# Kernel optimization log

Hardware: AMD Instinct MI355X
Metric: run time of the kernel (lower is better)

The kernel has to match this reference:

```python
import jax, jax.numpy as jnp
import numpy as np
from math import factorial

L_MAX = 3
K = 256
N = 2048


def _cg_coeff(l1, m1, l2, m2, l3, m3):
    # Clebsch-Gordan coefficient <l1 m1 l2 m2 | l3 m3> via the Racah formula.
    if m3 != m1 + m2:
        return 0.0
    pref = ((2 * l3 + 1) * factorial(l3 + l1 - l2) * factorial(l3 - l1 + l2)
            * factorial(l1 + l2 - l3) / factorial(l1 + l2 + l3 + 1)) ** 0.5
    pref *= (factorial(l3 + m3) * factorial(l3 - m3) * factorial(l1 - m1)
             * factorial(l1 + m1) * factorial(l2 - m2) * factorial(l2 + m2)) ** 0.5
    s = 0.0
    for k in range(0, l1 + l2 - l3 + 1):
        d = [k, l1 + l2 - l3 - k, l1 - m1 - k, l2 + m2 - k,
             l3 - l2 + m1 + k, l3 - l1 - m2 + k]
        if min(d) < 0:
            continue
        den = 1.0
        for x in d:
            den *= factorial(x)
        s += (-1.0) ** k / den
    return pref * s


def _cg_tensor(l1, l2, l3):
    out = np.zeros((2 * l1 + 1, 2 * l2 + 1, 2 * l3 + 1), dtype=np.float32)
    for m1 in range(-l1, l1 + 1):
        for m2 in range(-l2, l2 + 1):
            m3 = m1 + m2
            if -l3 <= m3 <= l3:
                out[m1 + l1, m2 + l2, m3 + l3] = _cg_coeff(l1, m1, l2, m2, l3, m3)
    return jnp.asarray(out)


# All (l1, l2) -> l coupling paths allowed by the triangle inequality, l <= L_MAX.
PATHS = {l: [(l1, l2) for l1 in range(L_MAX + 1) for l2 in range(L_MAX + 1)
             if abs(l1 - l2) <= l <= l1 + l2] for l in range(L_MAX + 1)}
CG = {(l1, l2, l): _cg_tensor(l1, l2, l)
      for l in range(L_MAX + 1) for (l1, l2) in PATHS[l]}


def _forward(f1, f2, U, W):
    outs = []
    for l in range(L_MAX + 1):
        # CG tensor product: elementwise over channels k, coupled over (m1, m2) -> m.
        parts = [jnp.einsum('abm,nak,nbk->nmk', CG[(l1, l2, l)], f1[l1], f2[l2])
                 for (l1, l2) in PATHS[l]]
        tp = jnp.concatenate(parts, axis=-1)          # [N, 2l+1, n_paths(l)*K]
        mixed = jnp.einsum('nmc,ck->nmk', tp, U[l])   # U_dict per-l mixing -> [N, 2l+1, K]
        mixed = jnp.einsum('nmk,kj->nmj', mixed, W[l])  # learned per-l linear
        outs.append(f1[l] + mixed)                    # residual
    return tuple(outs)


def setup_inputs() -> dict:
    key = jax.random.key(0)
    ks = jax.random.split(key, 16)
    inp = {}
    for l in range(L_MAX + 1):
        inp[f'f1_l{l}'] = jax.random.normal(ks[l], (N, 2 * l + 1, K), jnp.float32)
        inp[f'f2_l{l}'] = jax.random.normal(ks[4 + l], (N, 2 * l + 1, K), jnp.float32)
        cin = len(PATHS[l]) * K
        inp[f'U_{l}'] = jax.random.normal(ks[8 + l], (cin, K), jnp.float32) / float(np.sqrt(cin))
        inp[f'W_{l}'] = jax.random.normal(ks[12 + l], (K, K), jnp.float32) / float(np.sqrt(K))
    return inp


def reference(f1_l0, f1_l1, f1_l2, f1_l3,
              f2_l0, f2_l1, f2_l2, f2_l3,
              U_0, U_1, U_2, U_3,
              W_0, W_1, W_2, W_3):
    f1 = [f1_l0, f1_l1, f1_l2, f1_l3]
    f2 = [f2_l0, f2_l1, f2_l2, f2_l3]
    U = [U_0, U_1, U_2, U_3]
    W = [W_0, W_1, W_2, W_3]
    return _forward(f1, f2, U, W)
```

## Files before the change

kernel.cpp:

```cpp
#include <hip/hip_runtime.h>
#include <math.h>

typedef __attribute__((ext_vector_type(4))) float f32x4;
typedef __attribute__((ext_vector_type(8))) __bf16 bf16x8;
typedef __attribute__((ext_vector_type(4))) __bf16 bf16x4;

__device__ __constant__ int GP_L[34]  = {0,0,0,0, 1,1,1,1,1,1,1,1,1, 2,2,2,2,2,2,2,2,2,2,2, 3,3,3,3,3,3,3,3,3,3};
__device__ __constant__ int GP_L1[34] = {0,1,2,3, 0,1,1,1,2,2,2,3,3, 0,1,1,1,2,2,2,2,3,3,3, 0,1,1,2,2,2,3,3,3,3};
__device__ __constant__ int GP_L2[34] = {0,1,2,3, 1,0,1,2,1,2,3,2,3, 2,1,2,3,0,1,2,3,1,2,3, 3,2,3,1,2,3,0,1,2,3};

__device__ double dfact(int n) { double r = 1.0; for (int i = 2; i <= n; ++i) r *= (double)i; return r; }

__device__ double cg_coeff(int l1, int m1, int l2, int m2, int l3, int m3) {
  if (m3 != m1 + m2) return 0.0;
  double pref = sqrt((2.0 * l3 + 1.0) * dfact(l3 + l1 - l2) * dfact(l3 - l1 + l2)
                     * dfact(l1 + l2 - l3) / dfact(l1 + l2 + l3 + 1));
  pref *= sqrt(dfact(l3 + m3) * dfact(l3 - m3) * dfact(l1 - m1) * dfact(l1 + m1)
               * dfact(l2 - m2) * dfact(l2 + m2));
  double s = 0.0;
  for (int k = 0; k <= l1 + l2 - l3; ++k) {
    int d0 = k, d1 = l1 + l2 - l3 - k, d2 = l1 - m1 - k, d3 = l2 + m2 - k;
    int d4 = l3 - l2 + m1 + k, d5 = l3 - l1 - m2 + k;
    if (d0 < 0 || d1 < 0 || d2 < 0 || d3 < 0 || d4 < 0 || d5 < 0) continue;
    double den = dfact(d0) * dfact(d1) * dfact(d2) * dfact(d3) * dfact(d4) * dfact(d5);
    s += ((k & 1) ? -1.0 : 1.0) / den;
  }
  return pref * s;
}

__global__ void cg_init(float* __restrict__ cg) {
  int idx = blockIdx.x * 256 + threadIdx.x;
  if (idx >= 34 * 49) return;
  int gp = idx / 49, r = idx % 49;
  int m1i = r / 7, m2i = r % 7;
  int l3 = GP_L[gp], l1 = GP_L1[gp], l2 = GP_L2[gp];
  float v = 0.f;
  if (m1i <= 2 * l1 && m2i <= 2 * l2) {
    int m1 = m1i - l1, m2 = m2i - l2, m3 = m1 + m2;
    if (m3 >= -l3 && m3 <= l3) v = (float)cg_coeff(l1, m1, l2, m2, l3, m3);
  }
  cg[idx] = v;
}

__global__ __launch_bounds__(256) void cvt_u_all(
    const float* __restrict__ u0, const float* __restrict__ u1,
    const float* __restrict__ u2, const float* __restrict__ u3,
    __bf16* __restrict__ out) {
  long i = (long)blockIdx.x * 256 + threadIdx.x;
  const long b1 = 65536, b2 = 212992, b3 = 393216;
  const float* src; long s;
  if (i < b1)      { src = u0; s = i; }
  else if (i < b2) { src = u1; s = i - b1; }
  else if (i < b3) { src = u2; s = i - b2; }
  else             { src = u3; s = i - b3; }
  float4 v = ((const float4*)src)[s];
  bf16x4 o;
  o[0] = (__bf16)v.x; o[1] = (__bf16)v.y; o[2] = (__bf16)v.z; o[3] = (__bf16)v.w;
  ((bf16x4*)out)[i] = o;
}

__global__ void wt_cvt_all(const float* __restrict__ w0, const float* __restrict__ w1,
                           const float* __restrict__ w2, const float* __restrict__ w3,
                           __bf16* __restrict__ Wt) {
  int b = blockIdx.x;
  int l = b >> 8, j = b & 255, k = threadIdx.x;
  const float* W = (l == 0) ? w0 : (l == 1) ? w1 : (l == 2) ? w2 : w3;
  Wt[((long)l << 16) + (j << 8) + k] = (__bf16)W[(k << 8) + j];
}

template <int l1, int l2, int L>
__device__ __forceinline__ void tp_path2(const float* __restrict__ v1, const float* __restrict__ v2,
                                         const float* __restrict__ cgt, float* __restrict__ tp) {
#pragma unroll
  for (int a = 0; a < 2 * l1 + 1; ++a) {
#pragma unroll
    for (int b = 0; b < 2 * l2 + 1; ++b) {
      int mi = a + b - l1 - l2 + L;
      if (mi >= 0 && mi <= 2 * L)
        tp[mi] = fmaf(cgt[a * 7 + b], v1[a] * v2[b], tp[mi]);
    }
  }
}

#define TPW(LV, DST, CIN, GOFF, P, L1V, L2V)                                    \
  { float tp[2 * (LV) + 1] = {};                                                \
    tp_path2<L1V, L2V, LV>(v1 + CUM[L1V], v2 + CUM[L2V], cg + ((GOFF) + (P)) * 49, tp); \
    __bf16* o = (DST) + (n * (2 * (LV) + 1)) * (CIN) + (P) * 256 + k;           \
    _Pragma("unroll")                                                           \
    for (int m = 0; m < 2 * (LV) + 1; ++m) o[(long)m * (CIN)] = (__bf16)tp[m]; }

template <int LMASK>
__global__ __launch_bounds__(256) void tp_all(
    const float* __restrict__ f10, const float* __restrict__ f11,
    const float* __restrict__ f12, const float* __restrict__ f13,
    const float* __restrict__ f20, const float* __restrict__ f21,
    const float* __restrict__ f22, const float* __restrict__ f23,
    const float* __restrict__ cg,
    __bf16* __restrict__ A0, __bf16* __restrict__ A1,
    __bf16* __restrict__ A2, __bf16* __restrict__ A3) {
  const long n = blockIdx.x;
  const int k = threadIdx.x;
  constexpr int CUM[4] = {0, 1, 4, 9};
  const float* f1s[4] = {f10, f11, f12, f13};
  const float* f2s[4] = {f20, f21, f22, f23};

  float v1[16], v2[16];
#pragma unroll
  for (int l1 = 0; l1 < 4; ++l1) {
    const float* p1 = f1s[l1] + (n * (2 * l1 + 1)) * 256 + k;
    const float* p2 = f2s[l1] + (n * (2 * l1 + 1)) * 256 + k;
#pragma unroll
    for (int a = 0; a < 2 * l1 + 1; ++a) {
      v1[CUM[l1] + a] = p1[(long)a * 256];
      v2[CUM[l1] + a] = p2[(long)a * 256];
    }
  }

  if constexpr (LMASK & 1) {
    TPW(0, A0, 1024, 0, 0, 0, 0)  TPW(0, A0, 1024, 0, 1, 1, 1)
    TPW(0, A0, 1024, 0, 2, 2, 2)  TPW(0, A0, 1024, 0, 3, 3, 3)
  }
  if constexpr (LMASK & 2) {
    TPW(1, A1, 2304, 4, 0, 0, 1)  TPW(1, A1, 2304, 4, 1, 1, 0)
    TPW(1, A1, 2304, 4, 2, 1, 1)  TPW(1, A1, 2304, 4, 3, 1, 2)
    TPW(1, A1, 2304, 4, 4, 2, 1)  TPW(1, A1, 2304, 4, 5, 2, 2)
    TPW(1, A1, 2304, 4, 6, 2, 3)  TPW(1, A1, 2304, 4, 7, 3, 2)
    TPW(1, A1, 2304, 4, 8, 3, 3)
  }
  if constexpr (LMASK & 4) {
    TPW(2, A2, 2816, 13, 0, 0, 2)  TPW(2, A2, 2816, 13, 1, 1, 1)
    TPW(2, A2, 2816, 13, 2, 1, 2)  TPW(2, A2, 2816, 13, 3, 1, 3)
    TPW(2, A2, 2816, 13, 4, 2, 0)  TPW(2, A2, 2816, 13, 5, 2, 1)
    TPW(2, A2, 2816, 13, 6, 2, 2)  TPW(2, A2, 2816, 13, 7, 2, 3)
    TPW(2, A2, 2816, 13, 8, 3, 1)  TPW(2, A2, 2816, 13, 9, 3, 2)
    TPW(2, A2, 2816, 13, 10, 3, 3)
  }
  if constexpr (LMASK & 8) {
    TPW(3, A3, 2560, 24, 0, 0, 3)  TPW(3, A3, 2560, 24, 1, 1, 2)
    TPW(3, A3, 2560, 24, 2, 1, 3)  TPW(3, A3, 2560, 24, 3, 2, 1)
    TPW(3, A3, 2560, 24, 4, 2, 2)  TPW(3, A3, 2560, 24, 5, 2, 3)
    TPW(3, A3, 2560, 24, 6, 3, 0)  TPW(3, A3, 2560, 24, 7, 3, 1)
    TPW(3, A3, 2560, 24, 8, 3, 2)  TPW(3, A3, 2560, 24, 9, 3, 3)
  }
}

struct GemmDesc {
  const __bf16* A[4];
  const __bf16* B[4];
  void*         C[4];
  const float*  R[4];
  int start[4];
  int lmap[4];
  int Kd[4];
  int Nc[4];
};

__device__ __forceinline__ void gload_lds16(const void* g, void* l) {
  __builtin_amdgcn_global_load_lds((const __attribute__((address_space(1))) void*)g,
                                   (__attribute__((address_space(3))) void*)l, 16, 0, 0);
}

template <bool OUT_BF16, bool RESID>
__global__ __launch_bounds__(256) void gemm_batched(GemmDesc d) {
  __shared__ __bf16 As[128 * 64];
  __shared__ __bf16 Bs[128 * 64];
  const int tid = threadIdx.x;
  const int bid = blockIdx.x;
  int seg = 0;
  if (bid >= d.start[1]) seg = 1;
  if (bid >= d.start[2]) seg = 2;
  if (bid >= d.start[3]) seg = 3;
  const int l = d.lmap[seg];
  const int rel = bid - d.start[seg];
  const int Kd = d.Kd[l], Nc = d.Nc[l];
  const int nTN = Nc >> 7;
  const int tM = rel / nTN, tN = rel % nTN;

  const int lane = tid & 63, wave = tid >> 6;
  const int wm = (wave >> 1) << 6, wn = (wave & 1) << 6;
  const int lr = lane & 15, lk = (lane >> 4) << 3;

  f32x4 acc[4][4] = {};

  const int r32 = tid >> 3;
  const int sl = ((tid & 7) ^ (r32 & 7)) << 3;
  const __bf16* Ag = d.A[l] + (long)(tM * 128 + r32) * Kd + sl;
  const __bf16* Bg = d.B[l] + (long)(tN * 128 + r32) * Kd + sl;
  char* AsB = (char*)As;
  char* BsB = (char*)Bs;

  for (int kt = 0; kt < Kd; kt += 64) {
#pragma unroll
    for (int i = 0; i < 4; ++i) {
      gload_lds16(Ag + (long)i * 32 * Kd + kt, AsB + i * 4096 + tid * 16);
      gload_lds16(Bg + (long)i * 32 * Kd + kt, BsB + i * 4096 + tid * 16);
    }
    __syncthreads();

#pragma unroll
    for (int kk = 0; kk < 64; kk += 32) {
      bf16x8 af[4], bfr[4];
#pragma unroll
      for (int mi = 0; mi < 4; ++mi)
        af[mi] = *(const bf16x8*)(AsB + ((wm + mi * 16 + lr) << 7)
                                      + ((((kk + lk) << 1)) ^ ((lr & 7) << 4)));
#pragma unroll
      for (int ni = 0; ni < 4; ++ni)
        bfr[ni] = *(const bf16x8*)(BsB + ((wn + ni * 16 + lr) << 7)
                                       + ((((kk + lk) << 1)) ^ ((lr & 7) << 4)));
#pragma unroll
      for (int mi = 0; mi < 4; ++mi)
#pragma unroll
        for (int ni = 0; ni < 4; ++ni)
          acc[mi][ni] = __builtin_amdgcn_mfma_f32_16x16x32_bf16(af[mi], bfr[ni], acc[mi][ni], 0, 0, 0);
    }
    __syncthreads();
  }

  const long col0 = (long)tN * 128 + wn + lr;
  const long row0 = (long)tM * 128 + wm + ((lane >> 4) << 2);
#pragma unroll
  for (int mi = 0; mi < 4; ++mi) {
#pragma unroll
    for (int j = 0; j < 4; ++j) {
      long r = row0 + mi * 16 + j;
      long base = r * (long)Nc + col0;
#pragma unroll
      for (int ni = 0; ni < 4; ++ni) {
        long idx = base + ni * 16;
        float v = acc[mi][ni][j];
        if constexpr (RESID) v += d.R[l][idx];
        if constexpr (OUT_BF16) ((__bf16*)d.C[l])[idx] = (__bf16)v;
        else                    ((float*)d.C[l])[idx] = v;
      }
    }
  }
}

extern "C" void kernel_launch(void* const* d_in, const int* in_sizes, int n_in,
                              void* d_out, int out_size, void* d_ws, size_t ws_size,
                              hipStream_t stream) {
  const float* F1[4], * F2[4], * Uin[4], * Win[4];
  for (int l = 0; l < 4; ++l) {
    F1[l]  = (const float*)d_in[4 * l + 0];
    F2[l]  = (const float*)d_in[4 * l + 1];
    Uin[l] = (const float*)d_in[4 * l + 2];
    Win[l] = (const float*)d_in[4 * l + 3];
  }
  static const int  cin_[4]  = {1024, 2304, 2816, 2560};
  static const int  cum_[4]  = {0, 1024, 3328, 6144};
  static const long moff_[4] = {0, 524288, 2097152, 4718592};
  static const int  Ml_[4]   = {2048, 6144, 10240, 14336};
  static const long asz_[4]  = {4194304L, 28311552L, 57671680L, 73400320L};

  char* ws = (char*)d_ws;
  float*  cg   = (float*)ws;
  __bf16* Ubf  = (__bf16*)(ws + 8192);
  __bf16* Wtbf = (__bf16*)(ws + 8192 + 4456448);
  __bf16* UWt  = (__bf16*)(ws + 5242880);
  const long ABASE = 10485760;
  const bool big = ws_size >= (size_t)(ABASE + asz_[0] + asz_[1] + asz_[2] + asz_[3]);

  __bf16* Ab[4];
  if (big) {
    long off = ABASE;
    for (int l = 0; l < 4; ++l) { Ab[l] = (__bf16*)(ws + off); off += asz_[l]; }
  } else {
    for (int l = 0; l < 4; ++l) Ab[l] = (__bf16*)(ws + ABASE);
  }

  hipLaunchKernelGGL(cg_init, dim3(7), dim3(256), 0, stream, cg);
  hipLaunchKernelGGL(cvt_u_all, dim3(2176), dim3(256), 0, stream,
                     Uin[0], Uin[1], Uin[2], Uin[3], Ubf);
  hipLaunchKernelGGL(wt_cvt_all, dim3(1024), dim3(256), 0, stream,
                     Win[0], Win[1], Win[2], Win[3], Wtbf);

  {
    GemmDesc d;
    int starts[4] = {0, 40, 84, 120};
    int lmap[4]   = {3, 2, 1, 0};
    for (int s = 0; s < 4; ++s) { d.start[s] = starts[s]; d.lmap[s] = lmap[s]; }
    for (int l = 0; l < 4; ++l) {
      d.A[l] = Wtbf + (long)l * 65536;
      d.B[l] = Ubf + (long)cum_[l] * 256;
      d.C[l] = (void*)(UWt + (long)cum_[l] * 256);
      d.R[l] = nullptr;
      d.Kd[l] = 256;
      d.Nc[l] = cin_[l];
    }
    hipLaunchKernelGGL((gemm_batched<true, false>), dim3(136), dim3(256), 0, stream, d);
  }

  if (big) {
    hipLaunchKernelGGL((tp_all<15>), dim3(2048), dim3(256), 0, stream,
                       F1[0], F1[1], F1[2], F1[3], F2[0], F2[1], F2[2], F2[3],
                       cg, Ab[0], Ab[1], Ab[2], Ab[3]);
    GemmDesc d;
    int starts[4] = {0, 224, 384, 480};
    int lmap[4]   = {3, 2, 1, 0};
    for (int s = 0; s < 4; ++s) { d.start[s] = starts[s]; d.lmap[s] = lmap[s]; }
    for (int l = 0; l < 4; ++l) {
      d.A[l] = Ab[l];
      d.B[l] = UWt + (long)cum_[l] * 256;
      d.C[l] = (void*)((float*)d_out + moff_[l]);
      d.R[l] = F1[l];
      d.Kd[l] = cin_[l];
      d.Nc[l] = 256;
    }
    hipLaunchKernelGGL((gemm_batched<false, true>), dim3(512), dim3(256), 0, stream, d);
  } else {
    for (int l = 0; l < 4; ++l) {
      switch (l) {
        case 0: hipLaunchKernelGGL((tp_all<1>), dim3(2048), dim3(256), 0, stream,
                  F1[0],F1[1],F1[2],F1[3], F2[0],F2[1],F2[2],F2[3], cg,
                  Ab[0],Ab[1],Ab[2],Ab[3]); break;
        case 1: hipLaunchKernelGGL((tp_all<2>), dim3(2048), dim3(256), 0, stream,
                  F1[0],F1[1],F1[2],F1[3], F2[0],F2[1],F2[2],F2[3], cg,
                  Ab[0],Ab[1],Ab[2],Ab[3]); break;
        case 2: hipLaunchKernelGGL((tp_all<4>), dim3(2048), dim3(256), 0, stream,
                  F1[0],F1[1],F1[2],F1[3], F2[0],F2[1],F2[2],F2[3], cg,
                  Ab[0],Ab[1],Ab[2],Ab[3]); break;
        case 3: hipLaunchKernelGGL((tp_all<8>), dim3(2048), dim3(256), 0, stream,
                  F1[0],F1[1],F1[2],F1[3], F2[0],F2[1],F2[2],F2[3], cg,
                  Ab[0],Ab[1],Ab[2],Ab[3]); break;
      }
      GemmDesc d;
      for (int s = 0; s < 4; ++s) {
        d.start[s] = (s == 0) ? 0 : 0x7fffffff;
        d.lmap[s] = l;
      }
      for (int ll = 0; ll < 4; ++ll) {
        d.A[ll] = Ab[l];
        d.B[ll] = UWt + (long)cum_[l] * 256;
        d.C[ll] = (void*)((float*)d_out + moff_[l]);
        d.R[ll] = F1[l];
        d.Kd[ll] = cin_[l];
        d.Nc[ll] = 256;
      }
      hipLaunchKernelGGL((gemm_batched<false, true>), dim3((Ml_[l] >> 7) * 2), dim3(256),
                         0, stream, d);
    }
  }
  (void)in_sizes; (void)n_in; (void)out_size; (void)ws_size;
}
```

Measured before the change: 152.6 us.

## Add dedicated 128x256 double-buffered main GEMM, merge prep kernels, vectorize TP

Merges the three setup kernels (CG table, U conversion, W transpose) into one prep launch. Each tensor-product thread now handles two channels with float2 loads and bf16x2 stores, and the grid is halved. The main GEMM gets its own 512-thread kernel that computes a full 128x256 output tile per block, so the A panel is read once. It double-buffers LDS through global_load_lds with an XOR swizzle and remaps blocks across XCDs. This cuts launch overhead and re-reads of the large bf16 A matrix, at the cost of 96KB of LDS per block and only 256 blocks in the fused path.

```diff
diff --git a/kernel.cpp b/kernel.cpp
--- a/kernel.cpp
+++ b/kernel.cpp
@@ -2,8 +2,10 @@
 #include <math.h>
 
 typedef __attribute__((ext_vector_type(4))) float f32x4;
+typedef __attribute__((ext_vector_type(2))) float f32x2;
 typedef __attribute__((ext_vector_type(8))) __bf16 bf16x8;
 typedef __attribute__((ext_vector_type(4))) __bf16 bf16x4;
+typedef __attribute__((ext_vector_type(2))) __bf16 bf16x2;
 
 __device__ __constant__ int GP_L[34]  = {0,0,0,0, 1,1,1,1,1,1,1,1,1, 2,2,2,2,2,2,2,2,2,2,2, 3,3,3,3,3,3,3,3,3,3};
 __device__ __constant__ int GP_L1[34] = {0,1,2,3, 0,1,1,1,2,2,2,3,3, 0,1,1,1,2,2,2,2,3,3,3, 0,1,1,2,2,2,3,3,3,3};
@@ -28,119 +30,43 @@
   return pref * s;
 }
 
-__global__ void cg_init(float* __restrict__ cg) {
-  int idx = blockIdx.x * 256 + threadIdx.x;
-  if (idx >= 34 * 49) return;
-  int gp = idx / 49, r = idx % 49;
-  int m1i = r / 7, m2i = r % 7;
-  int l3 = GP_L[gp], l1 = GP_L1[gp], l2 = GP_L2[gp];
-  float v = 0.f;
-  if (m1i <= 2 * l1 && m2i <= 2 * l2) {
-    int m1 = m1i - l1, m2 = m2i - l2, m3 = m1 + m2;
-    if (m3 >= -l3 && m3 <= l3) v = (float)cg_coeff(l1, m1, l2, m2, l3, m3);
-  }
-  cg[idx] = v;
-}
-
-__global__ __launch_bounds__(256) void cvt_u_all(
+__global__ __launch_bounds__(256) void prep(
     const float* __restrict__ u0, const float* __restrict__ u1,
     const float* __restrict__ u2, const float* __restrict__ u3,
-    __bf16* __restrict__ out) {
-  long i = (long)blockIdx.x * 256 + threadIdx.x;
-  const long b1 = 65536, b2 = 212992, b3 = 393216;
-  const float* src; long s;
-  if (i < b1)      { src = u0; s = i; }
-  else if (i < b2) { src = u1; s = i - b1; }
-  else if (i < b3) { src = u2; s = i - b2; }
-  else             { src = u3; s = i - b3; }
-  float4 v = ((const float4*)src)[s];
-  bf16x4 o;
-  o[0] = (__bf16)v.x; o[1] = (__bf16)v.y; o[2] = (__bf16)v.z; o[3] = (__bf16)v.w;
-  ((bf16x4*)out)[i] = o;
-}
-
-__global__ void wt_cvt_all(const float* __restrict__ w0, const float* __restrict__ w1,
-                           const float* __restrict__ w2, const float* __restrict__ w3,
-                           __bf16* __restrict__ Wt) {
-  int b = blockIdx.x;
-  int l = b >> 8, j = b & 255, k = threadIdx.x;
-  const float* W = (l == 0) ? w0 : (l == 1) ? w1 : (l == 2) ? w2 : w3;
-  Wt[((long)l << 16) + (j << 8) + k] = (__bf16)W[(k << 8) + j];
-}
-
-template <int l1, int l2, int L>
-__device__ __forceinline__ void tp_path2(const float* __restrict__ v1, const float* __restrict__ v2,
-                                         const float* __restrict__ cgt, float* __restrict__ tp) {
-#pragma unroll
-  for (int a = 0; a < 2 * l1 + 1; ++a) {
-#pragma unroll
-    for (int b = 0; b < 2 * l2 + 1; ++b) {
-      int mi = a + b - l1 - l2 + L;
-      if (mi >= 0 && mi <= 2 * L)
-        tp[mi] = fmaf(cgt[a * 7 + b], v1[a] * v2[b], tp[mi]);
-    }
-  }
-}
-
-#define TPW(LV, DST, CIN, GOFF, P, L1V, L2V)                                    \
-  { float tp[2 * (LV) + 1] = {};                                                \
-    tp_path2<L1V, L2V, LV>(v1 + CUM[L1V], v2 + CUM[L2V], cg + ((GOFF) + (P)) * 49, tp); \
-    __bf16* o = (DST) + (n * (2 * (LV) + 1)) * (CIN) + (P) * 256 + k;           \
-    _Pragma("unroll")                                                           \
-    for (int m = 0; m < 2 * (LV) + 1; ++m) o[(long)m * (CIN)] = (__bf16)tp[m]; }
-
-template <int LMASK>
-__global__ __launch_bounds__(256) void tp_all(
-    const float* __restrict__ f10, const float* __restrict__ f11,
-    const float* __restrict__ f12, const float* __restrict__ f13,
-    const float* __restrict__ f20, const float* __restrict__ f21,
-    const float* __restrict__ f22, const float* __restrict__ f23,
-    const float* __restrict__ cg,
-    __bf16* __restrict__ A0, __bf16* __restrict__ A1,
-    __bf16* __restrict__ A2, __bf16* __restrict__ A3) {
-  const long n = blockIdx.x;
-  const int k = threadIdx.x;
-  constexpr int CUM[4] = {0, 1, 4, 9};
-  const float* f1s[4] = {f10, f11, f12, f13};
-  const float* f2s[4] = {f20, f21, f22, f23};
-
-  float v1[16], v2[16];
-#pragma unroll
-  for (int l1 = 0; l1 < 4; ++l1) {
-    const float* p1 = f1s[l1] + (n * (2 * l1 + 1)) * 256 + k;
-    const float* p2 = f2s[l1] + (n * (2 * l1 + 1)) * 256 + k;
-#pragma unroll
-    for (int a = 0; a < 2 * l1 + 1; ++a) {
-      v1[CUM[l1] + a] = p1[(long)a * 256];
-      v2[CUM[l1] + a] = p2[(long)a * 256];
-    }
-  }
-
-  if constexpr (LMASK & 1) {
-    TPW(0, A0, 1024, 0, 0, 0, 0)  TPW(0, A0, 1024, 0, 1, 1, 1)
-    TPW(0, A0, 1024, 0, 2, 2, 2)  TPW(0, A0, 1024, 0, 3, 3, 3)
-  }
-  if constexpr (LMASK & 2) {
-    TPW(1, A1, 2304, 4, 0, 0, 1)  TPW(1, A1, 2304, 4, 1, 1, 0)
-    TPW(1, A1, 2304, 4, 2, 1, 1)  TPW(1, A1, 2304, 4, 3, 1, 2)
-    TPW(1, A1, 2304, 4, 4, 2, 1)  TPW(1, A1, 2304, 4, 5, 2, 2)
-    TPW(1, A1, 2304, 4, 6, 2, 3)  TPW(1, A1, 2304, 4, 7, 3, 2)
-    TPW(1, A1, 2304, 4, 8, 3, 3)
-  }
-  if constexpr (LMASK & 4) {
-    TPW(2, A2, 2816, 13, 0, 0, 2)  TPW(2, A2, 2816, 13, 1, 1, 1)
-    TPW(2, A2, 2816, 13, 2, 1, 2)  TPW(2, A2, 2816, 13, 3, 1, 3)
-    TPW(2, A2, 2816, 13, 4, 2, 0)  TPW(2, A2, 2816, 13, 5, 2, 1)
-    TPW(2, A2, 2816, 13, 6, 2, 2)  TPW(2, A2, 2816, 13, 7, 2, 3)
-    TPW(2, A2, 2816, 13, 8, 3, 1)  TPW(2, A2, 2816, 13, 9, 3, 2)
-    TPW(2, A2, 2816, 13, 10, 3, 3)
-  }
-  if constexpr (LMASK & 8) {
-    TPW(3, A3, 2560, 24, 0, 0, 3)  TPW(3, A3, 2560, 24, 1, 1, 2)
-    TPW(3, A3, 2560, 24, 2, 1, 3)  TPW(3, A3, 2560, 24, 3, 2, 1)
-    TPW(3, A3, 2560, 24, 4, 2, 2)  TPW(3, A3, 2560, 24, 5, 2, 3)
-    TPW(3, A3, 2560, 24, 6, 3, 0)  TPW(3, A3, 2560, 24, 7, 3, 1)
-    TPW(3, A3, 2560, 24, 8, 3, 2)  TPW(3, A3, 2560, 24, 9, 3, 3)
+    const float* __restrict__ w0, const float* __restrict__ w1,
+    const float* __restrict__ w2, const float* __restrict__ w3,
+    __bf16* __restrict__ Ubf, __bf16* __restrict__ Wt, float* __restrict__ cg) {
+  const int bid = blockIdx.x, tid = threadIdx.x;
+  if (bid < 2176) {
+    long i = (long)bid * 256 + tid;
+    const long b1 = 65536, b2 = 212992, b3 = 393216;
+    const float* src; long s;
+    if (i < b1)      { src = u0; s = i; }
+    else if (i < b2) { src = u1; s = i - b1; }
+    else if (i < b3) { src = u2; s = i - b2; }
+    else             { src = u3; s = i - b3; }
+    float4 v = ((const float4*)src)[s];
+    bf16x4 o;
+    o[0] = (__bf16)v.x; o[1] = (__bf16)v.y; o[2] = (__bf16)v.z; o[3] = (__bf16)v.w;
+    ((bf16x4*)Ubf)[i] = o;
+  } else if (bid < 3200) {
+    int b = bid - 2176;
+    int l = b >> 8, j = b & 255;
+    const float* W = (l == 0) ? w0 : (l == 1) ? w1 : (l == 2) ? w2 : w3;
+    Wt[((long)l << 16) + (j << 8) + tid] = (__bf16)W[(tid << 8) + j];
+  } else {
+    int idx = (bid - 3200) * 256 + tid;
+    if (idx < 34 * 49) {
+      int gp = idx / 49, r = idx % 49;
+      int m1i = r / 7, m2i = r % 7;
+      int l3 = GP_L[gp], l1 = GP_L1[gp], l2 = GP_L2[gp];
+      float v = 0.f;
+      if (m1i <= 2 * l1 && m2i <= 2 * l2) {
+        int m1 = m1i - l1, m2 = m2i - l2, m3 = m1 + m2;
+        if (m3 >= -l3 && m3 <= l3) v = (float)cg_coeff(l1, m1, l2, m2, l3, m3);
+      }
+      cg[idx] = v;
+    }
   }
 }
 
@@ -148,7 +74,6 @@
   const __bf16* A[4];
   const __bf16* B[4];
   void*         C[4];
-  const float*  R[4];
   int start[4];
   int lmap[4];
   int Kd[4];
@@ -160,7 +85,6 @@
                                    (__attribute__((address_space(3))) void*)l, 16, 0, 0);
 }
 
-template <bool OUT_BF16, bool RESID>
 __global__ __launch_bounds__(256) void gemm_batched(GemmDesc d) {
   __shared__ __bf16 As[128 * 64];
   __shared__ __bf16 Bs[128 * 64];
@@ -226,15 +150,184 @@
       long r = row0 + mi * 16 + j;
       long base = r * (long)Nc + col0;
 #pragma unroll
+      for (int ni = 0; ni < 4; ++ni)
+        ((__bf16*)d.C[l])[base + ni * 16] = (__bf16)acc[mi][ni][j];
+    }
+  }
+}
+
+#define TPW2(LV, DST, CIN, GOFF, P, L1V, L2V)                                    \
+  { f32x2 tp[2 * (LV) + 1];                                                      \
+    _Pragma("unroll") for (int m = 0; m <= 2 * (LV); ++m) { tp[m][0] = 0.f; tp[m][1] = 0.f; } \
+    const float* cgt = cg + ((GOFF) + (P)) * 49;                                 \
+    _Pragma("unroll") for (int a = 0; a <= 2 * (L1V); ++a)                       \
+      _Pragma("unroll") for (int b = 0; b <= 2 * (L2V); ++b) {                   \
+        const int m = a + b - ((L1V) + (L2V) - (LV));                            \
+        if (m >= 0 && m <= 2 * (LV)) {                                           \
+          float c = cgt[a * 7 + b];                                              \
+          tp[m][0] = fmaf(c, v1[CUM[L1V] + a][0] * v2[CUM[L2V] + b][0], tp[m][0]); \
+          tp[m][1] = fmaf(c, v1[CUM[L1V] + a][1] * v2[CUM[L2V] + b][1], tp[m][1]); \
+        } }                                                                      \
+    __bf16* o = (DST) + (n * (2 * (LV) + 1)) * (CIN) + (P) * 256 + k2;           \
+    _Pragma("unroll") for (int m = 0; m <= 2 * (LV); ++m) {                      \
+      bf16x2 ov; ov[0] = (__bf16)tp[m][0]; ov[1] = (__bf16)tp[m][1];             \
+      *(bf16x2*)(o + (long)m * (CIN)) = ov; } }
+
+template <int LMASK>
+__global__ __launch_bounds__(256) void tp_all(
+    const float* __restrict__ f10, const float* __restrict__ f11,
+    const float* __restrict__ f12, const float* __restrict__ f13,
+    const float* __restrict__ f20, const float* __restrict__ f21,
+    const float* __restrict__ f22, const float* __restrict__ f23,
+    const float* __restrict__ cg,
+    __bf16* __restrict__ A0, __bf16* __restrict__ A1,
+    __bf16* __restrict__ A2, __bf16* __restrict__ A3) {
+  const int tid = threadIdx.x;
+  const long n = (long)blockIdx.x * 2 + (tid >> 7);
+  const int k2 = (tid & 127) << 1;
+  constexpr int CUM[4] = {0, 1, 4, 9};
+  const float* f1s[4] = {f10, f11, f12, f13};
+  const float* f2s[4] = {f20, f21, f22, f23};
+
+  f32x2 v1[16], v2[16];
+#pragma unroll
+  for (int l1 = 0; l1 < 4; ++l1) {
+    const float* p1 = f1s[l1] + (n * (2 * l1 + 1)) * 256 + k2;
+    const float* p2 = f2s[l1] + (n * (2 * l1 + 1)) * 256 + k2;
+#pragma unroll
+    for (int a = 0; a <= 2 * l1; ++a) {
+      v1[CUM[l1] + a] = *(const f32x2*)(p1 + (long)a * 256);
+      v2[CUM[l1] + a] = *(const f32x2*)(p2 + (long)a * 256);
+    }
+  }
+
+  if constexpr (LMASK & 1) {
+    TPW2(0, A0, 1024, 0, 0, 0, 0)  TPW2(0, A0, 1024, 0, 1, 1, 1)
+    TPW2(0, A0, 1024, 0, 2, 2, 2)  TPW2(0, A0, 1024, 0, 3, 3, 3)
+  }
+  if constexpr (LMASK & 2) {
+    TPW2(1, A1, 2304, 4, 0, 0, 1)  TPW2(1, A1, 2304, 4, 1, 1, 0)
+    TPW2(1, A1, 2304, 4, 2, 1, 1)  TPW2(1, A1, 2304, 4, 3, 1, 2)
+    TPW2(1, A1, 2304, 4, 4, 2, 1)  TPW2(1, A1, 2304, 4, 5, 2, 2)
+    TPW2(1, A1, 2304, 4, 6, 2, 3)  TPW2(1, A1, 2304, 4, 7, 3, 2)
+    TPW2(1, A1, 2304, 4, 8, 3, 3)
+  }
+  if constexpr (LMASK & 4) {
+    TPW2(2, A2, 2816, 13, 0, 0, 2)  TPW2(2, A2, 2816, 13, 1, 1, 1)
+    TPW2(2, A2, 2816, 13, 2, 1, 2)  TPW2(2, A2, 2816, 13, 3, 1, 3)
+    TPW2(2, A2, 2816, 13, 4, 2, 0)  TPW2(2, A2, 2816, 13, 5, 2, 1)
+    TPW2(2, A2, 2816, 13, 6, 2, 2)  TPW2(2, A2, 2816, 13, 7, 2, 3)
+    TPW2(2, A2, 2816, 13, 8, 3, 1)  TPW2(2, A2, 2816, 13, 9, 3, 2)
+    TPW2(2, A2, 2816, 13, 10, 3, 3)
+  }
+  if constexpr (LMASK & 8) {
+    TPW2(3, A3, 2560, 24, 0, 0, 3)  TPW2(3, A3, 2560, 24, 1, 1, 2)
+    TPW2(3, A3, 2560, 24, 2, 1, 3)  TPW2(3, A3, 2560, 24, 3, 2, 1)
+    TPW2(3, A3, 2560, 24, 4, 2, 2)  TPW2(3, A3, 2560, 24, 5, 2, 3)
+    TPW2(3, A3, 2560, 24, 6, 3, 0)  TPW2(3, A3, 2560, 24, 7, 3, 1)
+    TPW2(3, A3, 2560, 24, 8, 3, 2)  TPW2(3, A3, 2560, 24, 9, 3, 3)
+  }
+}
+
+struct MainDesc {
+  const __bf16* A[4];
+  const __bf16* B[4];
+  float*        C[4];
+  const float*  R[4];
+  int start[4];
+  int lmap[4];
+  int cin4[4];
+};
+
+__global__ __launch_bounds__(512) void gemm_main(MainDesc d) {
+  __shared__ __align__(16) char sm[98304];
+  const int tid = threadIdx.x;
+  int bid;
+  {
+    const int cpx = gridDim.x >> 3;
+    bid = (blockIdx.x & 7) * cpx + (blockIdx.x >> 3);
+  }
+  int seg = 0;
+  if (bid >= d.start[1]) seg = 1;
+  if (bid >= d.start[2]) seg = 2;
+  if (bid >= d.start[3]) seg = 3;
+  const int l = d.lmap[seg];
+  const int tM = bid - d.start[seg];
+  const int cin = d.cin4[l];
+  const int NT = cin >> 6;
+
+  const __bf16* __restrict__ Aseg = d.A[l] + (long)tM * 128 * cin;
+  const __bf16* __restrict__ Bseg = d.B[l];
+
+  const int srow = tid >> 3;
+  const int sx = ((tid & 7) ^ (srow & 7)) << 3;
+
+  f32x4 acc[4][4] = {};
+
+  const int lane = tid & 63, wave = tid >> 6;
+  const int wm = (wave >> 2) << 6;
+  const int wn = (wave & 3) << 6;
+  const int lr = lane & 15, lkb = (lane >> 4) << 3;
+
+#pragma unroll
+  for (int i = 0; i < 2; ++i)
+    gload_lds16(Aseg + (long)(i * 64 + srow) * cin + sx, sm + i * 8192 + tid * 16);
+#pragma unroll
+  for (int i = 0; i < 4; ++i)
+    gload_lds16(Bseg + (long)(i * 64 + srow) * cin + sx, sm + 32768 + i * 8192 + tid * 16);
+  __syncthreads();
+
+  for (int t = 0; t < NT; ++t) {
+    const int cur = t & 1;
+    if (t + 1 < NT) {
+      const int ktn = (t + 1) << 6;
+      char* An = sm + (cur ^ 1) * 16384;
+      char* Bn = sm + 32768 + (cur ^ 1) * 32768;
+#pragma unroll
+      for (int i = 0; i < 2; ++i)
+        gload_lds16(Aseg + (long)(i * 64 + srow) * cin + ktn + sx, An + i * 8192 + tid * 16);
+#pragma unroll
+      for (int i = 0; i < 4; ++i)
+        gload_lds16(Bseg + (long)(i * 64 + srow) * cin + ktn + sx, Bn + i * 8192 + tid * 16);
+    }
+    const char* Ab = sm + cur * 16384;
+    const char* Bb = sm + 32768 + cur * 32768;
+#pragma unroll
+    for (int kk = 0; kk < 64; kk += 32) {
+      bf16x8 af[4], bfr[4];
+#pragma unroll
+      for (int mi = 0; mi < 4; ++mi) {
+        const int row = wm + mi * 16 + lr;
+        af[mi] = *(const bf16x8*)(Ab + row * 128 + ((((kk + lkb) << 1)) ^ ((row & 7) << 4)));
+      }
+#pragma unroll
       for (int ni = 0; ni < 4; ++ni) {
-        long idx = base + ni * 16;
-        float v = acc[mi][ni][j];
-        if constexpr (RESID) v += d.R[l][idx];
-        if constexpr (OUT_BF16) ((__bf16*)d.C[l])[idx] = (__bf16)v;
-        else                    ((float*)d.C[l])[idx] = v;
-      }
-    }
-  }
+        const int row = wn + ni * 16 + lr;
+        bfr[ni] = *(const bf16x8*)(Bb + row * 128 + ((((kk + lkb) << 1)) ^ ((row & 7) << 4)));
+      }
+#pragma unroll
+      for (int mi = 0; mi < 4; ++mi)
+#pragma unroll
+        for (int ni = 0; ni < 4; ++ni)
+          acc[mi][ni] = __builtin_amdgcn_mfma_f32_16x16x32_bf16(af[mi], bfr[ni], acc[mi][ni], 0, 0, 0);
+    }
+    __syncthreads();
+  }
+
+  float* __restrict__ Cout = d.C[l];
+  const float* __restrict__ Resid = d.R[l];
+  const int col0 = wn + lr;
+  const int rb = (lane >> 4) << 2;
+#pragma unroll
+  for (int mi = 0; mi < 4; ++mi)
+#pragma unroll
+    for (int j = 0; j < 4; ++j) {
+      const long row = (long)tM * 128 + wm + mi * 16 + rb + j;
+      const long base = row * 256 + col0;
+#pragma unroll
+      for (int ni = 0; ni < 4; ++ni)
+        Cout[base + ni * 16] = acc[mi][ni][j] + Resid[base + ni * 16];
+    }
 }
 
 extern "C" void kernel_launch(void* const* d_in, const int* in_sizes, int n_in,
@@ -250,7 +343,7 @@
   static const int  cin_[4]  = {1024, 2304, 2816, 2560};
   static const int  cum_[4]  = {0, 1024, 3328, 6144};
   static const long moff_[4] = {0, 524288, 2097152, 4718592};
-  static const int  Ml_[4]   = {2048, 6144, 10240, 14336};
+  static const int  nTM_[4]  = {16, 48, 80, 112};
   static const long asz_[4]  = {4194304L, 28311552L, 57671680L, 73400320L};
 
   char* ws = (char*)d_ws;
@@ -269,11 +362,9 @@
     for (int l = 0; l < 4; ++l) Ab[l] = (__bf16*)(ws + ABASE);
   }
 
-  hipLaunchKernelGGL(cg_init, dim3(7), dim3(256), 0, stream, cg);
-  hipLaunchKernelGGL(cvt_u_all, dim3(2176), dim3(256), 0, stream,
-                     Uin[0], Uin[1], Uin[2], Uin[3], Ubf);
-  hipLaunchKernelGGL(wt_cvt_all, dim3(1024), dim3(256), 0, stream,
-                     Win[0], Win[1], Win[2], Win[3], Wtbf);
+  hipLaunchKernelGGL(prep, dim3(3207), dim3(256), 0, stream,
+                     Uin[0], Uin[1], Uin[2], Uin[3],
+                     Win[0], Win[1], Win[2], Win[3], Ubf, Wtbf, cg);
 
   {
     GemmDesc d;
@@ -284,47 +375,45 @@
       d.A[l] = Wtbf + (long)l * 65536;
       d.B[l] = Ubf + (long)cum_[l] * 256;
       d.C[l] = (void*)(UWt + (long)cum_[l] * 256);
-      d.R[l] = nullptr;
       d.Kd[l] = 256;
       d.Nc[l] = cin_[l];
     }
-    hipLaunchKernelGGL((gemm_batched<true, false>), dim3(136), dim3(256), 0, stream, d);
+    hipLaunchKernelGGL(gemm_batched, dim3(136), dim3(256), 0, stream, d);
   }
 
   if (big) {
-    hipLaunchKernelGGL((tp_all<15>), dim3(2048), dim3(256), 0, stream,
+    hipLaunchKernelGGL((tp_all<15>), dim3(1024), dim3(256), 0, stream,
                        F1[0], F1[1], F1[2], F1[3], F2[0], F2[1], F2[2], F2[3],
                        cg, Ab[0], Ab[1], Ab[2], Ab[3]);
-    GemmDesc d;
-    int starts[4] = {0, 224, 384, 480};
+    MainDesc d;
+    int starts[4] = {0, 112, 192, 240};
     int lmap[4]   = {3, 2, 1, 0};
     for (int s = 0; s < 4; ++s) { d.start[s] = starts[s]; d.lmap[s] = lmap[s]; }
     for (int l = 0; l < 4; ++l) {
       d.A[l] = Ab[l];
       d.B[l] = UWt + (long)cum_[l] * 256;
-      d.C[l] = (void*)((float*)d_out + moff_[l]);
+      d.C[l] = (float*)d_out + moff_[l];
       d.R[l] = F1[l];
-      d.Kd[l] = cin_[l];
-      d.Nc[l] = 256;
-    }
-    hipLaunchKernelGGL((gemm_batched<false, true>), dim3(512), dim3(256), 0, stream, d);
+      d.cin4[l] = cin_[l];
+    }
+    hipLaunchKernelGGL(gemm_main, dim3(256), dim3(512), 0, stream, d);
   } else {
     for (int l = 0; l < 4; ++l) {
       switch (l) {
-        case 0: hipLaunchKernelGGL((tp_all<1>), dim3(2048), dim3(256), 0, stream,
+        case 0: hipLaunchKernelGGL((tp_all<1>), dim3(1024), dim3(256), 0, stream,
                   F1[0],F1[1],F1[2],F1[3], F2[0],F2[1],F2[2],F2[3], cg,
                   Ab[0],Ab[1],Ab[2],Ab[3]); break;
-        case 1: hipLaunchKernelGGL((tp_all<2>), dim3(2048), dim3(256), 0, stream,
+        case 1: hipLaunchKernelGGL((tp_all<2>), dim3(1024), dim3(256), 0, stream,
                   F1[0],F1[1],F1[2],F1[3], F2[0],F2[1],F2[2],F2[3], cg,
                   Ab[0],Ab[1],Ab[2],Ab[3]); break;
-        case 2: hipLaunchKernelGGL((tp_all<4>), dim3(2048), dim3(256), 0, stream,
+        case 2: hipLaunchKernelGGL((tp_all<4>), dim3(1024), dim3(256), 0, stream,
                   F1[0],F1[1],F1[2],F1[3], F2[0],F2[1],F2[2],F2[3], cg,
                   Ab[0],Ab[1],Ab[2],Ab[3]); break;
-        case 3: hipLaunchKernelGGL((tp_all<8>), dim3(2048), dim3(256), 0, stream,
+        case 3: hipLaunchKernelGGL((tp_all<8>), dim3(1024), dim3(256), 0, stream,
                   F1[0],F1[1],F1[2],F1[3], F2[0],F2[1],F2[2],F2[3], cg,
                   Ab[0],Ab[1],Ab[2],Ab[3]); break;
       }
-      GemmDesc d;
+      MainDesc d;
       for (int s = 0; s < 4; ++s) {
         d.start[s] = (s == 0) ? 0 : 0x7fffffff;
         d.lmap[s] = l;
@@ -332,13 +421,11 @@
       for (int ll = 0; ll < 4; ++ll) {
         d.A[ll] = Ab[l];
         d.B[ll] = UWt + (long)cum_[l] * 256;
-        d.C[ll] = (void*)((float*)d_out + moff_[l]);
+        d.C[ll] = (float*)d_out + moff_[l];
         d.R[ll] = F1[l];
-        d.Kd[ll] = cin_[l];
-        d.Nc[ll] = 256;
-      }
-      hipLaunchKernelGGL((gemm_batched<false, true>), dim3((Ml_[l] >> 7) * 2), dim3(256),
-                         0, stream, d);
+        d.cin4[ll] = cin_[l];
+      }
+      hipLaunchKernelGGL(gemm_main, dim3(nTM_[l]), dim3(512), 0, stream, d);
     }
   }
   (void)in_sizes; (void)n_in; (void)out_size; (void)ws_size;
```

Result: faster. 135.2 us (-11.4%).
